# Performance work log

Measured on AMD Instinct MI355X. Metric: run time of the kernel, lower is better.

Reference implementation:

```python
import jax, jax.numpy as jnp
import numpy as np

SCORE_THRESH = 0.05
NMS_THRESH = 0.5
DETS_PER_IMG = 100
IMG_W, IMG_H = 1333.0, 800.0
BBOX_XFORM_CLIP = float(np.log(1000.0 / 16.0))
WX, WY, WW, WH = 10.0, 10.0, 5.0, 5.0


def decode_boxes(rel, ref):
    widths = ref[:, 2] - ref[:, 0] + 1.0
    heights = ref[:, 3] - ref[:, 1] + 1.0
    ctr_x = ref[:, 0] + 0.5 * widths
    ctr_y = ref[:, 1] + 0.5 * heights
    dx = rel[:, 0] / WX
    dy = rel[:, 1] / WY
    dw = jnp.minimum(rel[:, 2] / WW, BBOX_XFORM_CLIP)
    dh = jnp.minimum(rel[:, 3] / WH, BBOX_XFORM_CLIP)
    pcx = dx * widths + ctr_x
    pcy = dy * heights + ctr_y
    pw = jnp.exp(dw) * widths
    ph = jnp.exp(dh) * heights
    return jnp.stack([pcx - 0.5 * pw, pcy - 0.5 * ph,
                      pcx + 0.5 * pw - 1.0, pcy + 0.5 * ph - 1.0], axis=1)


def pairwise_iou(b):
    # torchvision-style IoU (no +1), b: [n,4] xyxy
    area = (b[:, 2] - b[:, 0]) * (b[:, 3] - b[:, 1])
    lt = jnp.maximum(b[:, None, :2], b[None, :, :2])
    rb = jnp.minimum(b[:, None, 2:], b[None, :, 2:])
    wh = jnp.clip(rb - lt, 0.0)
    inter = wh[..., 0] * wh[..., 1]
    return inter / (area[:, None] + area[None, :] - inter + 1e-12)


def nms_keep(boxes, scores, valid):
    # masked greedy NMS; returns boolean keep mask in original order
    n = boxes.shape[0]
    order = jnp.argsort(-jnp.where(valid, scores, -jnp.inf))
    b = boxes[order]
    v = valid[order]
    iou = pairwise_iou(b)  # [n,n]
    idx = jnp.arange(n)

    def body(i, keep):
        suppressed = jnp.any(keep & (iou[i] > NMS_THRESH) & (idx < i))
        return keep.at[i].set(v[i] & ~suppressed)

    keep_sorted = jax.lax.fori_loop(0, n, body, jnp.zeros(n, dtype=bool))
    return jnp.zeros(n, dtype=bool).at[order].set(keep_sorted)


def setup_inputs() -> dict:
    key = jax.random.key(0)
    k1, k2, k3, k4, k5 = jax.random.split(key, 5)
    C, K = 16, 2048
    class_logit = jax.random.normal(k1, (C * K, 2), jnp.float32)
    box_regression = jax.random.normal(k2, (C * K, 8), jnp.float32) * 0.5
    x1 = jax.random.uniform(k3, (K,)) * (IMG_W - 220.0)
    y1 = jax.random.uniform(k4, (K,)) * (IMG_H - 220.0)
    wh = 20.0 + jax.random.uniform(k5, (K, 2)) * 180.0
    proposal_boxes = jnp.stack([x1, y1, x1 + wh[:, 0], y1 + wh[:, 1]], axis=1).astype(jnp.float32)
    unique_labels = jnp.arange(1, C + 1, dtype=jnp.int32)
    return {"class_logit": class_logit, "box_regression": box_regression,
            "proposal_boxes": proposal_boxes, "unique_labels": unique_labels}


def reference(class_logit, box_regression, proposal_boxes, unique_labels):
    C = unique_labels.shape[0]
    K = proposal_boxes.shape[0]
    # softmax over binary logits, take foreground prob
    prob = jax.nn.softmax(class_logit, axis=1)[:, 1]  # [C*K]
    rel = box_regression[:, 4:8]
    ref_boxes = jnp.tile(proposal_boxes, (C, 1))  # class-major [C*K,4]
    dec = decode_boxes(rel, ref_boxes)
    # clip_to_image (remove_empty=False), TO_REMOVE = 1
    dec = jnp.stack([jnp.clip(dec[:, 0], 0.0, IMG_W - 1.0),
                     jnp.clip(dec[:, 1], 0.0, IMG_H - 1.0),
                     jnp.clip(dec[:, 2], 0.0, IMG_W - 1.0),
                     jnp.clip(dec[:, 3], 0.0, IMG_H - 1.0)], axis=1)
    boxes_c = dec.reshape(C, K, 4)
    scores_c = prob.reshape(C, K)
    valid = scores_c > SCORE_THRESH
    keep = jax.vmap(nms_keep)(boxes_c, scores_c, valid).reshape(-1)  # [C*K]
    flat_scores = scores_c.reshape(-1)
    n_det = jnp.sum(keep)
    masked = jnp.where(keep, flat_scores, -jnp.inf)
    kth = jax.lax.top_k(masked, DETS_PER_IMG)[0][-1]  # 100th largest kept score
    keep_final = jnp.where(n_det > DETS_PER_IMG, keep & (flat_scores >= kth), keep)
    labels = jnp.broadcast_to(unique_labels[:, None], (C, K)).reshape(-1)
    out_boxes = jnp.where(keep_final[:, None], dec, 0.0)
    out_scores = jnp.where(keep_final, flat_scores, 0.0)
    out5 = jnp.concatenate([out_boxes, out_scores[:, None]], axis=1)  # [C*K,5]
    return out5, labels, keep_final
```

## Files before the change

kernel.cpp:

```cpp
#include <hip/hip_runtime.h>
#include <hip/hip_bf16.h>

#define NCLS 16
#define NBOX 2048
#define NTOT (NCLS * NBOX)
#define NCHUNK 32
#define SCORE_THRESH 0.05f
#define NMS_THRESH 0.5f
#define DETS_PER_IMG 100
#define TOPC 128
#define BBOX_CLIP 4.135166556742356f

typedef unsigned long long u64;

__device__ __forceinline__ u64 sel_mx(u64 a, u64 b, bool keepmax) {
    u64 mx = (a > b) ? a : b;
    u64 mn = (a > b) ? b : a;
    return keepmax ? mx : mn;
}

__global__ __launch_bounds__(1024) void sortdecode_kernel(
    const float* __restrict__ logits,
    const float* __restrict__ regr,
    const float* __restrict__ props,
    float4* __restrict__ dec,
    u64* __restrict__ keys_out,
    float4* __restrict__ sbox4)
{
    int c = blockIdx.x;
    int tid = threadIdx.x;
    int w = tid >> 6, l = tid & 63;
    int p0 = w * 128 + l;
    int p1 = p0 + 64;
    __shared__ u64 sk[NBOX];

    u64 e01[2];
#pragma unroll
    for (int s = 0; s < 2; s++) {
#pragma clang fp contract(off)
        int t = s ? p1 : p0;
        int i = c * NBOX + t;
        float x0 = logits[2 * i + 0];
        float x1 = logits[2 * i + 1];
        float m = fmaxf(x0, x1);
        float e0f = expf(x0 - m);
        float e1f = expf(x1 - m);
        float score = e1f / (e0f + e1f);

        float px1 = props[4 * t + 0];
        float py1 = props[4 * t + 1];
        float px2 = props[4 * t + 2];
        float py2 = props[4 * t + 3];

        float bw = px2 - px1 + 1.0f;
        float bh = py2 - py1 + 1.0f;
        float cx = px1 + 0.5f * bw;
        float cy = py1 + 0.5f * bh;

        float dx = regr[8 * i + 4] / 10.0f;
        float dy = regr[8 * i + 5] / 10.0f;
        float dw = fminf(regr[8 * i + 6] / 5.0f, BBOX_CLIP);
        float dh = fminf(regr[8 * i + 7] / 5.0f, BBOX_CLIP);

        float pcx = dx * bw + cx;
        float pcy = dy * bh + cy;
        float pw  = expf(dw) * bw;
        float ph  = expf(dh) * bh;

        float b0 = pcx - 0.5f * pw;
        float b1 = pcy - 0.5f * ph;
        float b2 = pcx + 0.5f * pw - 1.0f;
        float b3 = pcy + 0.5f * ph - 1.0f;

        b0 = fminf(fmaxf(b0, 0.0f), 1332.0f);
        b1 = fminf(fmaxf(b1, 0.0f), 799.0f);
        b2 = fminf(fmaxf(b2, 0.0f), 1332.0f);
        b3 = fminf(fmaxf(b3, 0.0f), 799.0f);

        dec[i] = make_float4(b0, b1, b2, b3);

        unsigned mono = 0u;
        if (score > SCORE_THRESH) mono = __float_as_uint(score) | 0x80000000u;
        e01[s] = ((u64)mono << 32) | (u64)(unsigned)(NBOX - 1 - t);
    }
    u64 e0 = e01[0], e1 = e01[1];

    for (int k = 2; k <= NBOX; k <<= 1) {
        bool desc0 = (p0 & k) == 0;
        bool desc1 = (p1 & k) == 0;
        for (int j = k >> 1; j > 0; j >>= 1) {
            if (j >= 128) {
                sk[p0] = e0; sk[p1] = e1;
                __syncthreads();
                u64 q0 = sk[p0 ^ j];
                u64 q1 = sk[p1 ^ j];
                e0 = sel_mx(e0, q0, desc0 ^ ((p0 & j) != 0));
                e1 = sel_mx(e1, q1, desc1 ^ ((p1 & j) != 0));
                __syncthreads();
            } else if (j == 64) {
                u64 mx = (e0 > e1) ? e0 : e1;
                u64 mn = (e0 > e1) ? e1 : e0;
                e0 = desc0 ? mx : mn;
                e1 = desc0 ? mn : mx;
            } else {
                u64 q0 = __shfl_xor(e0, j);
                u64 q1 = __shfl_xor(e1, j);
                bool hi = (l & j) != 0;
                e0 = sel_mx(e0, q0, desc0 ^ hi);
                e1 = sel_mx(e1, q1, desc1 ^ hi);
            }
        }
    }

    sk[p0] = e0; sk[p1] = e1;
    __syncthreads();

    for (int t = tid; t < NBOX; t += 1024) {
        u64 key = sk[t];
        keys_out[c * NBOX + t] = key;
        int idx = (NBOX - 1) - (int)(key & 0xFFFFFFFFull);
        int orig = c * NBOX + idx;
        sbox4[c * NBOX + t] = dec[orig];
    }
}

__global__ __launch_bounds__(1024) void mask_kernel(
    const float4* __restrict__ sbox4,
    u64* __restrict__ maskT)
{
    int c = blockIdx.x >> 4;
    int p = blockIdx.x & 15;
    __shared__ float4 box[NBOX];

    for (int i = threadIdx.x; i < NBOX; i += 1024)
        box[i] = sbox4[c * NBOX + i];
    __syncthreads();

    int r = threadIdx.x & 63;
    int g = threadIdx.x >> 6;

    for (int pass = 0; pass < 2; pass++) {
#pragma clang fp contract(off)
        int Jc = pass ? (31 - p) : p;
        int j = Jc * 64 + r;
        float4 jb = box[j];
        float jar = (jb.z - jb.x) * (jb.w - jb.y);
        float hj = 0.5f * jar;
        float colC = hj + 5e-13f;

        for (int I = g; I <= Jc; I += 16) {
            u64 w = 0;
            int rbase = I * 64;
#pragma unroll
            for (int i2 = 0; i2 < 64; i2++) {
#pragma clang fp contract(off)
                int gi = rbase + i2;
                float4 rb = box[gi];
                float ar = (rb.z - rb.x) * (rb.w - rb.y);
                float rha = 0.5f * ar;
                float lx = fmaxf(rb.x, jb.x);
                float ly = fmaxf(rb.y, jb.y);
                float rx = fminf(rb.z, jb.z);
                float ry = fminf(rb.w, jb.w);
                float ww = fmaxf(rx - lx, 0.0f);
                float hh = fmaxf(ry - ly, 0.0f);
                float inter = ww * hh;
                float s  = rha + colC;
                float band = 2e-6f * s;
                float delta = fmaf(1.5f, inter, -s);
                bool over = delta > band;
                bool amb = fabsf(delta) <= band;
                if (__any(amb)) {
                    float un = ar + jar - inter + 1e-12f;
                    float iou = inter / un;
                    bool ovx = iou > NMS_THRESH;
                    over = amb ? ovx : over;
                }
                if (over) w |= 1ull << i2;
            }
            if (I == Jc) w &= (1ull << r) - 1ull;
            maskT[((size_t)c * NCHUNK + I) * NBOX + j] = w;
        }
    }
}

__global__ __launch_bounds__(64) void resolve_kernel(
    const u64* __restrict__ keys,
    const u64* __restrict__ maskT,
    unsigned* __restrict__ keepbits,
    unsigned* __restrict__ compact,
    int* __restrict__ nkept)
{
    int c = blockIdx.x;
    int l = threadIdx.x;
    const u64* MT = maskT + (size_t)c * NCHUNK * NBOX;
    const u64* K  = keys + (size_t)c * NBOX;

    unsigned sup = 0;
    int offset = 0;
    u64 tm[2][NCHUNK - 1];

#pragma unroll
    for (int t = 0; t < NCHUNK - 1; t++)
        tm[0][t] = MT[(size_t)(1 + t) * 64 + l];
    u64 diag = MT[l];
    u64 key  = K[l];

#pragma unroll
    for (int I = 0; I < NCHUNK; I++) {
        u64 diagN = diag, keyN = key;
        if (I + 1 < NCHUNK) {
            const u64* rowpN = MT + (size_t)(I + 1) * NBOX + l;
#pragma unroll
            for (int t = 0; t < NCHUNK - 2 - I; t++)
                tm[(I + 1) & 1][t] = rowpN[(size_t)(I + 2 + t) * 64];
            diagN = MT[(size_t)(I + 1) * NBOX + (size_t)(I + 1) * 64 + l];
            keyN  = K[(I + 1) * 64 + l];
        }
        __builtin_amdgcn_sched_barrier(0);

        unsigned mono = (unsigned)(key >> 32);
        bool av = (mono != 0u) && (((sup >> I) & 1u) == 0u);
        u64 kept = 0;
        u64 availB = __ballot(av);
        while (availB) {
            u64 front = __ballot(av && ((diag & availB) == 0ull));
            kept |= front;
            bool fr = ((front >> l) & 1ull) != 0ull;
            bool sp = ((diag & front) != 0ull);
            av = av && !fr && !sp;
            availB = __ballot(av);
        }

        int idx = (NBOX - 1) - (int)(key & 0xFFFFFFFFull);
        bool isk = ((kept >> l) & 1ull) != 0ull;
        keepbits[c * NBOX + idx] = isk ? (mono & 0x7FFFFFFFu) : 0u;

        int pos = offset + __popcll(kept & ((1ull << l) - 1ull));
        if (isk && pos < TOPC) compact[c * TOPC + pos] = mono;
        offset += __popcll(kept);

#pragma unroll
        for (int t = 0; t < NCHUNK - 1 - I; t++)
            sup |= (tm[I & 1][t] & kept) ? (1u << (I + 1 + t)) : 0u;

        diag = diagN;
        key  = keyN;
    }

    for (int t = offset + l; t < TOPC; t += 64) compact[c * TOPC + t] = 0u;
    if (l == 0) nkept[c] = offset;
}

__global__ __launch_bounds__(64) void select_kernel(
    const unsigned* __restrict__ compact,
    const int* __restrict__ nkept,
    int* __restrict__ stats)
{
    __shared__ unsigned ls[NCLS * TOPC];
    int l = threadIdx.x;

    for (int t = l; t < NCLS * TOPC; t += 64) ls[t] = compact[t];
    int n_c = (l < NCLS) ? nkept[l] : 0;
    __syncthreads();

    int nd = n_c;
#pragma unroll
    for (int off = 32; off > 0; off >>= 1) nd += __shfl_down(nd, off);
    nd = __shfl(nd, 0);

    unsigned kth = 0u;
    if (nd > DETS_PER_IMG) {
        const unsigned* my = &ls[(l & 15) * TOPC];
        bool active = (l < NCLS);
        unsigned prefix = 0u;
        for (int bit = 31; bit >= 0; bit--) {
            unsigned cand = prefix | (1u << bit);
            int cnt = 0;
            if (active) {
                if (my[TOPC - 1] >= cand) cnt = TOPC;
                else {
                    int pos = 0;
#pragma unroll
                    for (int step = 64; step >= 1; step >>= 1)
                        if (my[pos + step - 1] >= cand) pos += step;
                    cnt = pos;
                }
            }
#pragma unroll
            for (int off = 32; off > 0; off >>= 1) cnt += __shfl_down(cnt, off);
            cnt = __shfl(cnt, 0);
            if (cnt >= DETS_PER_IMG) prefix = cand;
        }
        kth = prefix & 0x7FFFFFFFu;
    }

    if (l == 0) {
        stats[0] = nd;
        stats[1] = (int)kth;
    }
}

__global__ __launch_bounds__(256) void write_kernel(
    const unsigned* __restrict__ keepbits,
    const float4* __restrict__ dec,
    const int* __restrict__ stats,
    const int* __restrict__ ulabels,
    float* __restrict__ out)
{
    int i = blockIdx.x * blockDim.x + threadIdx.x;
    if (i >= NTOT) return;

    int n_det = stats[0];
    unsigned kth = (unsigned)stats[1];
    unsigned kb = keepbits[i];
    bool kf = kb && (n_det <= DETS_PER_IMG || kb >= kth);

    float4 b = dec[i];
    float* o5 = out + (size_t)i * 5;
    if (kf) {
        o5[0] = b.x; o5[1] = b.y; o5[2] = b.z; o5[3] = b.w;
        o5[4] = __uint_as_float(kb);
    } else {
        o5[0] = 0.0f; o5[1] = 0.0f; o5[2] = 0.0f; o5[3] = 0.0f; o5[4] = 0.0f;
    }

    int c = i >> 11;
    out[NTOT * 5 + i] = (float)ulabels[c];
    out[NTOT * 5 + NTOT + i] = kf ? 1.0f : 0.0f;
}

extern "C" void kernel_launch(void* const* d_in, const int* in_sizes, int n_in,
                              void* d_out, int out_size, void* d_ws, size_t ws_size,
                              hipStream_t stream) {
    (void)in_sizes; (void)n_in; (void)out_size; (void)ws_size;

    const float* class_logit    = (const float*)d_in[0];
    const float* box_regression = (const float*)d_in[1];
    const float* proposal_boxes = (const float*)d_in[2];
    const int*   unique_labels  = (const int*)d_in[3];

    char* ws = (char*)d_ws;
    float4* dec        = (float4*)(ws + 0);
    u64* keys          = (u64*)(ws + 524288);
    float4* sbox4      = (float4*)(ws + 786432);
    unsigned* keepbits = (unsigned*)(ws + 1441792);
    int* stats         = (int*)(ws + 1572864);
    u64* maskT         = (u64*)(ws + 1573120);
    unsigned* compact  = (unsigned*)(ws + 9961728);
    int* nkept         = (int*)(ws + 9969920);

    float* out = (float*)d_out;

    sortdecode_kernel<<<NCLS, 1024, 0, stream>>>(class_logit, box_regression,
                                                 proposal_boxes, dec, keys,
                                                 sbox4);
    mask_kernel<<<NCLS * 16, 1024, 0, stream>>>(sbox4, maskT);
    resolve_kernel<<<NCLS, 64, 0, stream>>>(keys, maskT, keepbits,
                                            compact, nkept);
    select_kernel<<<1, 64, 0, stream>>>(compact, nkept, stats);
    write_kernel<<<NTOT / 256, 256, 0, stream>>>(keepbits, dec, stats,
                                                 unique_labels, out);
}
```

Measured before the change: 144.4 us.

## Fuse sort/decode into mask kernel and fold select/write into resolve

The sort/decode step is now recomputed redundantly by all 16 mask blocks per class, so the sorted boxes come straight from shared memory with no global round trip and one fewer launch. The select and write kernels are folded into the resolve kernel. The last block to finish, detected with an atomic counter, computes the top-k threshold, and the other blocks spin on a flag before each writes its own class's outputs. This removes three kernel launches and the keepbits/sbox global buffers. The costs are 16x redundant softmax/decode/bitonic sort work, much higher shared memory use (about 80KB per block), and an inter-block spin wait that depends on all 16 blocks being resident at once.

After: 149.9 us. 1.04x slower.

```diff
diff --git a/kernel.cpp b/kernel.cpp
--- a/kernel.cpp
+++ b/kernel.cpp
@@ -19,20 +19,27 @@
     return keepmax ? mx : mn;
 }
 
-__global__ __launch_bounds__(1024) void sortdecode_kernel(
+__global__ __launch_bounds__(1024) void sortmask_kernel(
     const float* __restrict__ logits,
     const float* __restrict__ regr,
     const float* __restrict__ props,
     float4* __restrict__ dec,
     u64* __restrict__ keys_out,
-    float4* __restrict__ sbox4)
+    u64* __restrict__ maskT,
+    int* __restrict__ flags)
 {
-    int c = blockIdx.x;
+    int blk = blockIdx.x;
+    int c = blk >> 4;
+    int p = blk & 15;
     int tid = threadIdx.x;
+    if (blk == 0 && tid == 0) { flags[0] = 0; flags[1] = 0; }
+
     int w = tid >> 6, l = tid & 63;
     int p0 = w * 128 + l;
     int p1 = p0 + 64;
     __shared__ u64 sk[NBOX];
+    __shared__ float4 decv[NBOX];
+    __shared__ float4 box[NBOX];
 
     u64 e01[2];
 #pragma unroll
@@ -77,7 +84,9 @@
         b2 = fminf(fmaxf(b2, 0.0f), 1332.0f);
         b3 = fminf(fmaxf(b3, 0.0f), 799.0f);
 
-        dec[i] = make_float4(b0, b1, b2, b3);
+        float4 bb = make_float4(b0, b1, b2, b3);
+        decv[t] = bb;
+        if (p == 0) dec[i] = bb;
 
         unsigned mono = 0u;
         if (score > SCORE_THRESH) mono = __float_as_uint(score) | 0x80000000u;
@@ -117,27 +126,14 @@
 
     for (int t = tid; t < NBOX; t += 1024) {
         u64 key = sk[t];
-        keys_out[c * NBOX + t] = key;
+        if (p == 0) keys_out[c * NBOX + t] = key;
         int idx = (NBOX - 1) - (int)(key & 0xFFFFFFFFull);
-        int orig = c * NBOX + idx;
-        sbox4[c * NBOX + t] = dec[orig];
-    }
-}
-
-__global__ __launch_bounds__(1024) void mask_kernel(
-    const float4* __restrict__ sbox4,
-    u64* __restrict__ maskT)
-{
-    int c = blockIdx.x >> 4;
-    int p = blockIdx.x & 15;
-    __shared__ float4 box[NBOX];
-
-    for (int i = threadIdx.x; i < NBOX; i += 1024)
-        box[i] = sbox4[c * NBOX + i];
+        box[t] = decv[idx];
+    }
     __syncthreads();
 
-    int r = threadIdx.x & 63;
-    int g = threadIdx.x >> 6;
+    int r = tid & 63;
+    int g = tid >> 6;
 
     for (int pass = 0; pass < 2; pass++) {
 #pragma clang fp contract(off)
@@ -149,7 +145,7 @@
         float colC = hj + 5e-13f;
 
         for (int I = g; I <= Jc; I += 16) {
-            u64 w = 0;
+            u64 wm = 0;
             int rbase = I * 64;
 #pragma unroll
             for (int i2 = 0; i2 < 64; i2++) {
@@ -176,10 +172,10 @@
                     bool ovx = iou > NMS_THRESH;
                     over = amb ? ovx : over;
                 }
-                if (over) w |= 1ull << i2;
+                if (over) wm |= 1ull << i2;
             }
-            if (I == Jc) w &= (1ull << r) - 1ull;
-            maskT[((size_t)c * NCHUNK + I) * NBOX + j] = w;
+            if (I == Jc) wm &= (1ull << r) - 1ull;
+            maskT[((size_t)c * NCHUNK + I) * NBOX + j] = wm;
         }
     }
 }
@@ -187,14 +183,21 @@
 __global__ __launch_bounds__(64) void resolve_kernel(
     const u64* __restrict__ keys,
     const u64* __restrict__ maskT,
-    unsigned* __restrict__ keepbits,
+    const float4* __restrict__ dec,
+    const int* __restrict__ ulabels,
     unsigned* __restrict__ compact,
-    int* __restrict__ nkept)
+    int* __restrict__ nkept,
+    int* __restrict__ stats,
+    int* __restrict__ flags,
+    float* __restrict__ out)
 {
     int c = blockIdx.x;
     int l = threadIdx.x;
     const u64* MT = maskT + (size_t)c * NCHUNK * NBOX;
     const u64* K  = keys + (size_t)c * NBOX;
+
+    __shared__ unsigned keep_lds[NBOX];
+    __shared__ unsigned ls[NCLS * TOPC];
 
     unsigned sup = 0;
     int offset = 0;
@@ -234,7 +237,7 @@
 
         int idx = (NBOX - 1) - (int)(key & 0xFFFFFFFFull);
         bool isk = ((kept >> l) & 1ull) != 0ull;
-        keepbits[c * NBOX + idx] = isk ? (mono & 0x7FFFFFFFu) : 0u;
+        keep_lds[idx] = isk ? (mono & 0x7FFFFFFFu) : 0u;
 
         int pos = offset + __popcll(kept & ((1ull << l) - 1ull));
         if (isk && pos < TOPC) compact[c * TOPC + pos] = mono;
@@ -250,84 +253,84 @@
 
     for (int t = offset + l; t < TOPC; t += 64) compact[c * TOPC + t] = 0u;
     if (l == 0) nkept[c] = offset;
-}
-
-__global__ __launch_bounds__(64) void select_kernel(
-    const unsigned* __restrict__ compact,
-    const int* __restrict__ nkept,
-    int* __restrict__ stats)
-{
-    __shared__ unsigned ls[NCLS * TOPC];
-    int l = threadIdx.x;
-
-    for (int t = l; t < NCLS * TOPC; t += 64) ls[t] = compact[t];
-    int n_c = (l < NCLS) ? nkept[l] : 0;
     __syncthreads();
-
-    int nd = n_c;
-#pragma unroll
-    for (int off = 32; off > 0; off >>= 1) nd += __shfl_down(nd, off);
-    nd = __shfl(nd, 0);
-
-    unsigned kth = 0u;
-    if (nd > DETS_PER_IMG) {
-        const unsigned* my = &ls[(l & 15) * TOPC];
-        bool active = (l < NCLS);
-        unsigned prefix = 0u;
-        for (int bit = 31; bit >= 0; bit--) {
-            unsigned cand = prefix | (1u << bit);
-            int cnt = 0;
-            if (active) {
-                if (my[TOPC - 1] >= cand) cnt = TOPC;
-                else {
-                    int pos = 0;
-#pragma unroll
-                    for (int step = 64; step >= 1; step >>= 1)
-                        if (my[pos + step - 1] >= cand) pos += step;
-                    cnt = pos;
+    __threadfence();
+
+    int got = 0;
+    if (l == 0) got = atomicAdd(&flags[0], 1);
+    got = __shfl(got, 0);
+
+    if (got == NCLS - 1) {
+        __threadfence();
+        for (int t = l; t < NCLS * TOPC; t += 64) ls[t] = compact[t];
+        int n_c = (l < NCLS) ? nkept[l] : 0;
+        __syncthreads();
+
+        int nd = n_c;
+#pragma unroll
+        for (int off = 32; off > 0; off >>= 1) nd += __shfl_down(nd, off);
+        nd = __shfl(nd, 0);
+
+        unsigned kth = 0u;
+        if (nd > DETS_PER_IMG) {
+            const unsigned* my = &ls[(l & 15) * TOPC];
+            bool active = (l < NCLS);
+            unsigned prefix = 0u;
+            for (int bit = 31; bit >= 0; bit--) {
+                unsigned cand = prefix | (1u << bit);
+                int cnt = 0;
+                if (active) {
+                    if (my[TOPC - 1] >= cand) cnt = TOPC;
+                    else {
+                        int pos = 0;
+#pragma unroll
+                        for (int step = 64; step >= 1; step >>= 1)
+                            if (my[pos + step - 1] >= cand) pos += step;
+                        cnt = pos;
+                    }
                 }
+#pragma unroll
+                for (int off = 32; off > 0; off >>= 1) cnt += __shfl_down(cnt, off);
+                cnt = __shfl(cnt, 0);
+                if (cnt >= DETS_PER_IMG) prefix = cand;
             }
-#pragma unroll
-            for (int off = 32; off > 0; off >>= 1) cnt += __shfl_down(cnt, off);
-            cnt = __shfl(cnt, 0);
-            if (cnt >= DETS_PER_IMG) prefix = cand;
-        }
-        kth = prefix & 0x7FFFFFFFu;
-    }
-
-    if (l == 0) {
-        stats[0] = nd;
-        stats[1] = (int)kth;
-    }
-}
-
-__global__ __launch_bounds__(256) void write_kernel(
-    const unsigned* __restrict__ keepbits,
-    const float4* __restrict__ dec,
-    const int* __restrict__ stats,
-    const int* __restrict__ ulabels,
-    float* __restrict__ out)
-{
-    int i = blockIdx.x * blockDim.x + threadIdx.x;
-    if (i >= NTOT) return;
+            kth = prefix & 0x7FFFFFFFu;
+        }
+
+        if (l == 0) {
+            stats[0] = nd;
+            stats[1] = (int)kth;
+            __threadfence();
+            __hip_atomic_store(&flags[1], 1, __ATOMIC_RELEASE,
+                               __HIP_MEMORY_SCOPE_AGENT);
+        }
+        __syncthreads();
+    } else {
+        if (l == 0) {
+            while (__hip_atomic_load(&flags[1], __ATOMIC_ACQUIRE,
+                                     __HIP_MEMORY_SCOPE_AGENT) == 0) {}
+        }
+        __syncthreads();
+    }
 
     int n_det = stats[0];
     unsigned kth = (unsigned)stats[1];
-    unsigned kb = keepbits[i];
-    bool kf = kb && (n_det <= DETS_PER_IMG || kb >= kth);
-
-    float4 b = dec[i];
-    float* o5 = out + (size_t)i * 5;
-    if (kf) {
-        o5[0] = b.x; o5[1] = b.y; o5[2] = b.z; o5[3] = b.w;
-        o5[4] = __uint_as_float(kb);
-    } else {
-        o5[0] = 0.0f; o5[1] = 0.0f; o5[2] = 0.0f; o5[3] = 0.0f; o5[4] = 0.0f;
-    }
-
-    int c = i >> 11;
-    out[NTOT * 5 + i] = (float)ulabels[c];
-    out[NTOT * 5 + NTOT + i] = kf ? 1.0f : 0.0f;
+    float lab = (float)ulabels[c];
+    for (int t = l; t < NBOX; t += 64) {
+        unsigned kb = keep_lds[t];
+        bool kf = kb && (n_det <= DETS_PER_IMG || kb >= kth);
+        int i = c * NBOX + t;
+        float4 b = dec[i];
+        float* o5 = out + (size_t)i * 5;
+        if (kf) {
+            o5[0] = b.x; o5[1] = b.y; o5[2] = b.z; o5[3] = b.w;
+            o5[4] = __uint_as_float(kb);
+        } else {
+            o5[0] = 0.0f; o5[1] = 0.0f; o5[2] = 0.0f; o5[3] = 0.0f; o5[4] = 0.0f;
+        }
+        out[NTOT * 5 + i] = lab;
+        out[NTOT * 5 + NTOT + i] = kf ? 1.0f : 0.0f;
+    }
 }
 
 extern "C" void kernel_launch(void* const* d_in, const int* in_sizes, int n_in,
@@ -343,22 +346,17 @@
     char* ws = (char*)d_ws;
     float4* dec        = (float4*)(ws + 0);
     u64* keys          = (u64*)(ws + 524288);
-    float4* sbox4      = (float4*)(ws + 786432);
-    unsigned* keepbits = (unsigned*)(ws + 1441792);
-    int* stats         = (int*)(ws + 1572864);
-    u64* maskT         = (u64*)(ws + 1573120);
-    unsigned* compact  = (unsigned*)(ws + 9961728);
-    int* nkept         = (int*)(ws + 9969920);
+    u64* maskT         = (u64*)(ws + 786432);
+    unsigned* compact  = (unsigned*)(ws + 9175040);
+    int* nkept         = (int*)(ws + 9183232);
+    int* stats         = (int*)(ws + 9183296);
+    int* flags         = (int*)(ws + 9183360);
 
     float* out = (float*)d_out;
 
-    sortdecode_kernel<<<NCLS, 1024, 0, stream>>>(class_logit, box_regression,
-                                                 proposal_boxes, dec, keys,
-                                                 sbox4);
-    mask_kernel<<<NCLS * 16, 1024, 0, stream>>>(sbox4, maskT);
-    resolve_kernel<<<NCLS, 64, 0, stream>>>(keys, maskT, keepbits,
-                                            compact, nkept);
-    select_kernel<<<1, 64, 0, stream>>>(compact, nkept, stats);
-    write_kernel<<<NTOT / 256, 256, 0, stream>>>(keepbits, dec, stats,
-                                                 unique_labels, out);
+    sortmask_kernel<<<NCLS * 16, 1024, 0, stream>>>(class_logit, box_regression,
+                                                    proposal_boxes, dec, keys,
+                                                    maskT, flags);
+    resolve_kernel<<<NCLS, 64, 0, stream>>>(keys, maskT, dec, unique_labels,
+                                            compact, nkept, stats, flags, out);
 }
```
